# Performance work log

Measured on AMD Instinct MI355X. Metric: run time of the kernel, lower is better.

## Reference

```python
import jax, jax.numpy as jnp
import numpy as np

WINDOW_SIZE = 11
SIGMA = 1.5
C1 = 0.01 ** 2
C2 = 0.03 ** 2


def _gaussian_window(channels):
    coords = jnp.arange(WINDOW_SIZE, dtype=jnp.float32) - WINDOW_SIZE // 2
    g = jnp.exp(-coords ** 2 / (2.0 * SIGMA ** 2))
    g = g / g.sum()
    w2d = g[:, None] * g[None, :]                      # [K, K]
    # depthwise kernel: [out_ch=C, in_ch/groups=1, K, K]
    return jnp.broadcast_to(w2d[None, None], (channels, 1, WINDOW_SIZE, WINDOW_SIZE))


def _depthwise_conv(x, window):
    # x: [B, C, H, W]; grouped conv with feature_group_count = C, SAME padding
    C = x.shape[1]
    pad = WINDOW_SIZE // 2
    return jax.lax.conv_general_dilated(
        x, window,
        window_strides=(1, 1),
        padding=((pad, pad), (pad, pad)),
        dimension_numbers=("NCHW", "OIHW", "NCHW"),
        feature_group_count=C,
    )


def setup_inputs() -> dict:
    key = jax.random.key(0)
    k1, k2 = jax.random.split(key)
    shape = (16, 3, 512, 512)
    pred = jax.random.uniform(k1, shape, dtype=jnp.float32)
    target = jax.random.uniform(k2, shape, dtype=jnp.float32)
    return {"pred": pred, "target": target}


def reference(pred, target):
    C = pred.shape[1]
    window = _gaussian_window(C)
    mu_p = _depthwise_conv(pred, window)
    mu_t = _depthwise_conv(target, window)
    mu_p_sq = mu_p ** 2
    mu_t_sq = mu_t ** 2
    mu_cross = mu_p * mu_t
    sigma_p_sq = _depthwise_conv(pred ** 2, window) - mu_p_sq
    sigma_t_sq = _depthwise_conv(target ** 2, window) - mu_t_sq
    sigma_cross = _depthwise_conv(pred * target, window) - mu_cross
    ssim_map = ((2.0 * mu_cross + C1) * (2.0 * sigma_cross + C2)) / (
        (mu_p_sq + mu_t_sq + C1) * (sigma_p_sq + sigma_t_sq + C2)
    )
    return 1.0 - ssim_map.mean()
```

## Files before the change

### kernel.cpp

```cpp
#include <hip/hip_runtime.h>

#define HH 512
#define WW 512
#define NPLANE 48
#define BY 128
#define CHK 16
#define NCH (BY / CHK)
#define SLOTS 40
#define KS 11

typedef __attribute__((ext_vector_type(8))) short short8;
typedef __attribute__((ext_vector_type(4))) float floatx4;
typedef __attribute__((ext_vector_type(2))) float float2v;
typedef __attribute__((ext_vector_type(2))) __bf16 bf16x2v;

__device__ inline unsigned pk2bf_rne(float a, float b) {
    union { float f; unsigned u; } ua, ub;
    ua.f = a; ub.f = b;
    unsigned lo = (ua.u + 0x7FFFu + ((ua.u >> 16) & 1u)) >> 16;
    unsigned hi = (ub.u + 0x7FFFu + ((ub.u >> 16) & 1u)) >> 16;
    return lo | (hi << 16);
}

__device__ inline unsigned pkbf(float a, float b) {
    float2v f = {a, b};
    bf16x2v v = __builtin_convertvector(f, bf16x2v);
    return __builtin_bit_cast(unsigned, v);
}

struct Raw { float4 p0, p1, t0, t1; };

__global__ __launch_bounds__(256, 4) void ssim_kernel(
    const float* __restrict__ pred, const float* __restrict__ target,
    float* __restrict__ ws_sum)
{
    __shared__ __align__(16) short ring[4][4][16][SLOTS];

    const int tid = threadIdx.x;
    const int wv = tid >> 6;
    const int lane = tid & 63;
    const int m = lane & 15;
    const int quad = lane >> 4;

    float wsum = 0.f;
#pragma unroll
    for (int k = 0; k < KS; ++k) {
        float d = (float)(k - 5);
        wsum += __expf(-d * d * (1.0f / 4.5f));
    }
    const float invs = 1.0f / wsum;

    short8 Wf;
    {
        union { short8 v; unsigned u[4]; } W;
#pragma unroll
        for (int jj = 0; jj < 4; ++jj) {
            float v0, v1;
            {
                int idx = quad * 8 + 2 * jj - m - 3;
                float d = (float)(idx - 5);
                v0 = (idx >= 0 && idx < KS) ? __expf(-d * d * (1.0f / 4.5f)) * invs : 0.f;
            }
            {
                int idx = quad * 8 + 2 * jj + 1 - m - 3;
                float d = (float)(idx - 5);
                v1 = (idx >= 0 && idx < KS) ? __expf(-d * d * (1.0f / 4.5f)) * invs : 0.f;
            }
            W.u[jj] = pk2bf_rne(v0, v1);
        }
        Wf = W.v;
    }

    const size_t poff = (size_t)blockIdx.z * HH * WW;
    const float* __restrict__ pp = pred + poff;
    const float* __restrict__ tp = target + poff;
    const int X0 = blockIdx.x * 64 + wv * 16;
    const int rawX = X0 - 8;
    const int Y0 = blockIdx.y * BY;

    const float C1 = 1.0e-4f;
    const float C2 = 9.0e-4f;
    float lsum = 0.f;
    const floatx4 z = {0.f, 0.f, 0.f, 0.f};

    auto load_raw = [&](int k) -> Raw {
        Raw r;
        r.p0 = make_float4(0, 0, 0, 0); r.p1 = make_float4(0, 0, 0, 0);
        r.t0 = make_float4(0, 0, 0, 0); r.t1 = make_float4(0, 0, 0, 0);
        const int row = Y0 + CHK * k - 8 + m;
        if ((unsigned)row < (unsigned)HH) {
            const float* pr = pp + (size_t)row * WW;
            const float* tr = tp + (size_t)row * WW;
            const int c0 = rawX + quad * 8;
            if ((unsigned)c0 < (unsigned)WW) {
                r.p0 = *(const float4*)(pr + c0);
                r.t0 = *(const float4*)(tr + c0);
            }
            if ((unsigned)(c0 + 4) < (unsigned)WW) {
                r.p1 = *(const float4*)(pr + c0 + 4);
                r.t1 = *(const float4*)(tr + c0 + 4);
            }
        }
        return r;
    };

    auto h_step = [&](const Raw& r, int sb) {
        const float p[8] = {r.p0.x, r.p0.y, r.p0.z, r.p0.w,
                            r.p1.x, r.p1.y, r.p1.z, r.p1.w};
        const float t[8] = {r.t0.x, r.t0.y, r.t0.z, r.t0.w,
                            r.t1.x, r.t1.y, r.t1.z, r.t1.w};
        union { short8 v; unsigned u[4]; } Fp, Ft, Fq, Fpt;
#pragma unroll
        for (int jj = 0; jj < 4; ++jj) {
            const float a0 = p[2 * jj], a1 = p[2 * jj + 1];
            const float b0 = t[2 * jj], b1 = t[2 * jj + 1];
            Fp.u[jj]  = pkbf(a0, a1);
            Ft.u[jj]  = pkbf(b0, b1);
            Fq.u[jj]  = pkbf(fmaf(a0, a0, b0 * b0), fmaf(a1, a1, b1 * b1));
            Fpt.u[jj] = pkbf(a0 * b0, a1 * b1);
        }
        floatx4 Dp  = __builtin_amdgcn_mfma_f32_16x16x32_bf16(Fp.v,  Wf, z, 0, 0, 0);
        floatx4 Dt  = __builtin_amdgcn_mfma_f32_16x16x32_bf16(Ft.v,  Wf, z, 0, 0, 0);
        floatx4 Dq  = __builtin_amdgcn_mfma_f32_16x16x32_bf16(Fq.v,  Wf, z, 0, 0, 0);
        floatx4 Dpt = __builtin_amdgcn_mfma_f32_16x16x32_bf16(Fpt.v, Wf, z, 0, 0, 0);
        int slot = sb + quad * 4;
        if (slot >= SLOTS) slot -= SLOTS;
        uint2 v;
        v.x = pkbf(Dp[0], Dp[1]);   v.y = pkbf(Dp[2], Dp[3]);
        *(uint2*)&ring[wv][0][m][slot] = v;
        v.x = pkbf(Dt[0], Dt[1]);   v.y = pkbf(Dt[2], Dt[3]);
        *(uint2*)&ring[wv][1][m][slot] = v;
        v.x = pkbf(Dq[0], Dq[1]);   v.y = pkbf(Dq[2], Dq[3]);
        *(uint2*)&ring[wv][2][m][slot] = v;
        v.x = pkbf(Dpt[0], Dpt[1]); v.y = pkbf(Dpt[2], Dpt[3]);
        *(uint2*)&ring[wv][3][m][slot] = v;
    };

    Raw A = load_raw(0);
    Raw B = load_raw(1);
    Raw C = load_raw(2);
    Raw D = load_raw(3);
    h_step(A, (0 * CHK + SLOTS - 8) % SLOTS);
    h_step(B, (1 * CHK + SLOTS - 8) % SLOTS);
    int hb = (2 * CHK + SLOTS - 8) % SLOTS;
    int vb = SLOTS - 8;
#pragma unroll 1
    for (int i = 0; i < NCH; ++i) {
        int sq = vb + quad * 8;
        if (sq >= SLOTS) sq -= SLOTS;
        const short8 Bp  = *(const short8*)&ring[wv][0][m][sq];
        const short8 Bt  = *(const short8*)&ring[wv][1][m][sq];
        const short8 Bq  = *(const short8*)&ring[wv][2][m][sq];
        const short8 Bpt = *(const short8*)&ring[wv][3][m][sq];
        vb += CHK; if (vb >= SLOTS) vb -= SLOTS;

        if (i + 2 <= NCH) {
            h_step(C, hb);
            hb += CHK; if (hb >= SLOTS) hb -= SLOTS;
            C = D;
        }
        if (i + 4 <= NCH) D = load_raw(i + 4);

        floatx4 Mp  = __builtin_amdgcn_mfma_f32_16x16x32_bf16(Wf, Bp,  z, 0, 0, 0);
        floatx4 Mt  = __builtin_amdgcn_mfma_f32_16x16x32_bf16(Wf, Bt,  z, 0, 0, 0);
        floatx4 Mq  = __builtin_amdgcn_mfma_f32_16x16x32_bf16(Wf, Bq,  z, 0, 0, 0);
        floatx4 Mpt = __builtin_amdgcn_mfma_f32_16x16x32_bf16(Wf, Bpt, z, 0, 0, 0);
#pragma unroll
        for (int r = 0; r < 4; ++r) {
            const float mup = Mp[r], mut = Mt[r];
            const float mupsq = mup * mup, mutsq = mut * mut, mucr = mup * mut;
            const float scr = Mpt[r] - mucr;
            const float n1 = 2.f * mucr + C1;
            const float n2 = 2.f * scr + C2;
            const float d1 = mupsq + mutsq + C1;
            const float d2 = (Mq[r] - mupsq - mutsq) + C2;
            lsum += __fdividef(n1 * n2, d1 * d2);
        }
    }

#pragma unroll
    for (int off = 32; off > 0; off >>= 1) lsum += __shfl_down(lsum, off, 64);
    if (lane == 0) *(float*)&ring[wv][0][0][0] = lsum;
    __syncthreads();
    if (tid == 0) {
        atomicAdd(ws_sum, *(const float*)&ring[0][0][0][0]
                        + *(const float*)&ring[1][0][0][0]
                        + *(const float*)&ring[2][0][0][0]
                        + *(const float*)&ring[3][0][0][0]);
    }
}

__global__ void finalize_kernel(const float* __restrict__ ws_sum,
                                float* __restrict__ out) {
    out[0] = 1.0f - ws_sum[0] * (1.0f / 12582912.0f);
}

extern "C" void kernel_launch(void* const* d_in, const int* in_sizes, int n_in,
                              void* d_out, int out_size, void* d_ws, size_t ws_size,
                              hipStream_t stream) {
    const float* pred = (const float*)d_in[0];
    const float* target = (const float*)d_in[1];
    float* out = (float*)d_out;
    float* ws = (float*)d_ws;

    hipMemsetAsync(ws, 0, sizeof(float), stream);
    dim3 grid(WW / 64, HH / BY, NPLANE);
    ssim_kernel<<<grid, 256, 0, stream>>>(pred, target, ws);
    finalize_kernel<<<1, 1, 0, stream>>>(ws, out);
}
```

Before: 141.5 us.

## Shrink LDS ring to power-of-two, unroll pipeline by two, pack float2 math

Reduces the per-wave LDS ring from 40 to 32 slots so slot indices use a mask instead of a compare-and-subtract, and raises the launch-bounds occupancy hint from 4 to 6 blocks. The main loop is unrolled by two with fixed ring offsets and explicit prologue and epilogue steps, and row/column address and bounds checks are hoisted. The elementwise products and the SSIM epilogue now use float2 vector operations, so the compiler can emit packed FP32 instructions. The tighter register budget from the higher occupancy hint could cause spills, and the smaller ring must still leave room for every row the vertical pass reads.

```diff
diff --git a/kernel.cpp b/kernel.cpp
--- a/kernel.cpp
+++ b/kernel.cpp
@@ -6,7 +6,7 @@
 #define BY 128
 #define CHK 16
 #define NCH (BY / CHK)
-#define SLOTS 40
+#define SLOTS 32
 #define KS 11
 
 typedef __attribute__((ext_vector_type(8))) short short8;
@@ -22,15 +22,14 @@
     return lo | (hi << 16);
 }
 
-__device__ inline unsigned pkbf(float a, float b) {
-    float2v f = {a, b};
+__device__ inline unsigned pkbf2(float2v f) {
     bf16x2v v = __builtin_convertvector(f, bf16x2v);
     return __builtin_bit_cast(unsigned, v);
 }
 
 struct Raw { float4 p0, p1, t0, t1; };
 
-__global__ __launch_bounds__(256, 4) void ssim_kernel(
+__global__ __launch_bounds__(256, 6) void ssim_kernel(
     const float* __restrict__ pred, const float* __restrict__ target,
     float* __restrict__ ws_sum)
 {
@@ -72,14 +71,18 @@
     }
 
     const size_t poff = (size_t)blockIdx.z * HH * WW;
-    const float* __restrict__ pp = pred + poff;
-    const float* __restrict__ tp = target + poff;
     const int X0 = blockIdx.x * 64 + wv * 16;
     const int rawX = X0 - 8;
     const int Y0 = blockIdx.y * BY;
 
-    const float C1 = 1.0e-4f;
-    const float C2 = 9.0e-4f;
+    const int c0 = rawX + quad * 8;
+    const bool okc0 = (unsigned)c0 < (unsigned)WW;
+    const bool okc1 = (unsigned)(c0 + 4) < (unsigned)WW;
+    const float* __restrict__ pc = pred + poff + c0;
+    const float* __restrict__ tc = target + poff + c0;
+
+    const float2v C1v = {1.0e-4f, 1.0e-4f};
+    const float2v C2v = {9.0e-4f, 9.0e-4f};
     float lsum = 0.f;
     const floatx4 z = {0.f, 0.f, 0.f, 0.f};
 
@@ -89,94 +92,100 @@
         r.t0 = make_float4(0, 0, 0, 0); r.t1 = make_float4(0, 0, 0, 0);
         const int row = Y0 + CHK * k - 8 + m;
         if ((unsigned)row < (unsigned)HH) {
-            const float* pr = pp + (size_t)row * WW;
-            const float* tr = tp + (size_t)row * WW;
-            const int c0 = rawX + quad * 8;
-            if ((unsigned)c0 < (unsigned)WW) {
-                r.p0 = *(const float4*)(pr + c0);
-                r.t0 = *(const float4*)(tr + c0);
-            }
-            if ((unsigned)(c0 + 4) < (unsigned)WW) {
-                r.p1 = *(const float4*)(pr + c0 + 4);
-                r.t1 = *(const float4*)(tr + c0 + 4);
-            }
+            const float* pr = pc + (size_t)row * WW;
+            const float* tr = tc + (size_t)row * WW;
+            if (okc0) { r.p0 = *(const float4*)pr;      r.t0 = *(const float4*)tr; }
+            if (okc1) { r.p1 = *(const float4*)(pr + 4); r.t1 = *(const float4*)(tr + 4); }
         }
         return r;
     };
 
     auto h_step = [&](const Raw& r, int sb) {
-        const float p[8] = {r.p0.x, r.p0.y, r.p0.z, r.p0.w,
-                            r.p1.x, r.p1.y, r.p1.z, r.p1.w};
-        const float t[8] = {r.t0.x, r.t0.y, r.t0.z, r.t0.w,
-                            r.t1.x, r.t1.y, r.t1.z, r.t1.w};
+        const float2v pa[4] = {{r.p0.x, r.p0.y}, {r.p0.z, r.p0.w},
+                               {r.p1.x, r.p1.y}, {r.p1.z, r.p1.w}};
+        const float2v tb[4] = {{r.t0.x, r.t0.y}, {r.t0.z, r.t0.w},
+                               {r.t1.x, r.t1.y}, {r.t1.z, r.t1.w}};
         union { short8 v; unsigned u[4]; } Fp, Ft, Fq, Fpt;
 #pragma unroll
         for (int jj = 0; jj < 4; ++jj) {
-            const float a0 = p[2 * jj], a1 = p[2 * jj + 1];
-            const float b0 = t[2 * jj], b1 = t[2 * jj + 1];
-            Fp.u[jj]  = pkbf(a0, a1);
-            Ft.u[jj]  = pkbf(b0, b1);
-            Fq.u[jj]  = pkbf(fmaf(a0, a0, b0 * b0), fmaf(a1, a1, b1 * b1));
-            Fpt.u[jj] = pkbf(a0 * b0, a1 * b1);
+            Fp.u[jj]  = pkbf2(pa[jj]);
+            Ft.u[jj]  = pkbf2(tb[jj]);
+            Fq.u[jj]  = pkbf2(pa[jj] * pa[jj] + tb[jj] * tb[jj]);
+            Fpt.u[jj] = pkbf2(pa[jj] * tb[jj]);
         }
         floatx4 Dp  = __builtin_amdgcn_mfma_f32_16x16x32_bf16(Fp.v,  Wf, z, 0, 0, 0);
         floatx4 Dt  = __builtin_amdgcn_mfma_f32_16x16x32_bf16(Ft.v,  Wf, z, 0, 0, 0);
         floatx4 Dq  = __builtin_amdgcn_mfma_f32_16x16x32_bf16(Fq.v,  Wf, z, 0, 0, 0);
         floatx4 Dpt = __builtin_amdgcn_mfma_f32_16x16x32_bf16(Fpt.v, Wf, z, 0, 0, 0);
-        int slot = sb + quad * 4;
-        if (slot >= SLOTS) slot -= SLOTS;
+        const int slot = (sb + quad * 4) & (SLOTS - 1);
         uint2 v;
-        v.x = pkbf(Dp[0], Dp[1]);   v.y = pkbf(Dp[2], Dp[3]);
+        v.x = pkbf2(float2v{Dp[0],  Dp[1]});  v.y = pkbf2(float2v{Dp[2],  Dp[3]});
         *(uint2*)&ring[wv][0][m][slot] = v;
-        v.x = pkbf(Dt[0], Dt[1]);   v.y = pkbf(Dt[2], Dt[3]);
+        v.x = pkbf2(float2v{Dt[0],  Dt[1]});  v.y = pkbf2(float2v{Dt[2],  Dt[3]});
         *(uint2*)&ring[wv][1][m][slot] = v;
-        v.x = pkbf(Dq[0], Dq[1]);   v.y = pkbf(Dq[2], Dq[3]);
+        v.x = pkbf2(float2v{Dq[0],  Dq[1]});  v.y = pkbf2(float2v{Dq[2],  Dq[3]});
         *(uint2*)&ring[wv][2][m][slot] = v;
-        v.x = pkbf(Dpt[0], Dpt[1]); v.y = pkbf(Dpt[2], Dpt[3]);
+        v.x = pkbf2(float2v{Dpt[0], Dpt[1]}); v.y = pkbf2(float2v{Dpt[2], Dpt[3]});
         *(uint2*)&ring[wv][3][m][slot] = v;
     };
 
-    Raw A = load_raw(0);
-    Raw B = load_raw(1);
-    Raw C = load_raw(2);
-    Raw D = load_raw(3);
-    h_step(A, (0 * CHK + SLOTS - 8) % SLOTS);
-    h_step(B, (1 * CHK + SLOTS - 8) % SLOTS);
-    int hb = (2 * CHK + SLOTS - 8) % SLOTS;
-    int vb = SLOTS - 8;
-#pragma unroll 1
-    for (int i = 0; i < NCH; ++i) {
-        int sq = vb + quad * 8;
-        if (sq >= SLOTS) sq -= SLOTS;
-        const short8 Bp  = *(const short8*)&ring[wv][0][m][sq];
-        const short8 Bt  = *(const short8*)&ring[wv][1][m][sq];
-        const short8 Bq  = *(const short8*)&ring[wv][2][m][sq];
-        const short8 Bpt = *(const short8*)&ring[wv][3][m][sq];
-        vb += CHK; if (vb >= SLOTS) vb -= SLOTS;
-
-        if (i + 2 <= NCH) {
-            h_step(C, hb);
-            hb += CHK; if (hb >= SLOTS) hb -= SLOTS;
-            C = D;
-        }
-        if (i + 4 <= NCH) D = load_raw(i + 4);
-
+    short8 Bp, Bt, Bq, Bpt;
+    auto vread = [&](int base) {
+        const int sq = (base + quad * 8) & (SLOTS - 1);
+        Bp  = *(const short8*)&ring[wv][0][m][sq];
+        Bt  = *(const short8*)&ring[wv][1][m][sq];
+        Bq  = *(const short8*)&ring[wv][2][m][sq];
+        Bpt = *(const short8*)&ring[wv][3][m][sq];
+    };
+
+    auto vfin = [&]() {
         floatx4 Mp  = __builtin_amdgcn_mfma_f32_16x16x32_bf16(Wf, Bp,  z, 0, 0, 0);
         floatx4 Mt  = __builtin_amdgcn_mfma_f32_16x16x32_bf16(Wf, Bt,  z, 0, 0, 0);
         floatx4 Mq  = __builtin_amdgcn_mfma_f32_16x16x32_bf16(Wf, Bq,  z, 0, 0, 0);
         floatx4 Mpt = __builtin_amdgcn_mfma_f32_16x16x32_bf16(Wf, Bpt, z, 0, 0, 0);
 #pragma unroll
-        for (int r = 0; r < 4; ++r) {
-            const float mup = Mp[r], mut = Mt[r];
-            const float mupsq = mup * mup, mutsq = mut * mut, mucr = mup * mut;
-            const float scr = Mpt[r] - mucr;
-            const float n1 = 2.f * mucr + C1;
-            const float n2 = 2.f * scr + C2;
-            const float d1 = mupsq + mutsq + C1;
-            const float d2 = (Mq[r] - mupsq - mutsq) + C2;
-            lsum += __fdividef(n1 * n2, d1 * d2);
-        }
-    }
+        for (int h = 0; h < 2; ++h) {
+            const float2v mup = {Mp[2*h],  Mp[2*h+1]};
+            const float2v mut = {Mt[2*h],  Mt[2*h+1]};
+            const float2v mq  = {Mq[2*h],  Mq[2*h+1]};
+            const float2v mpt = {Mpt[2*h], Mpt[2*h+1]};
+            const float2v mupsq = mup * mup, mutsq = mut * mut, mucr = mup * mut;
+            const float2v scr = mpt - mucr;
+            const float2v n1 = mucr + mucr + C1v;
+            const float2v n2 = scr + scr + C2v;
+            const float2v d1 = mupsq + mutsq + C1v;
+            const float2v d2 = (mq - mupsq - mutsq) + C2v;
+            const float2v num = n1 * n2, den = d1 * d2;
+            lsum += __fdividef(num[0], den[0]) + __fdividef(num[1], den[1]);
+        }
+    };
+
+    {
+        Raw A = load_raw(0);
+        Raw B = load_raw(1);
+        h_step(A, 24);
+        h_step(B, 8);
+    }
+    Raw C = load_raw(2);
+    Raw D = load_raw(3);
+
+#pragma unroll 1
+    for (int ii = 0; ii < 6; ii += 2) {
+        vread(24);
+        h_step(C, 24);
+        C = load_raw(ii + 4);
+        vfin();
+
+        vread(8);
+        h_step(D, 8);
+        if (ii < 4) D = load_raw(ii + 5);
+        vfin();
+    }
+    vread(24);
+    h_step(C, 24);
+    vfin();
+    vread(8);
+    vfin();
 
 #pragma unroll
     for (int off = 32; off > 0; off >>= 1) lsum += __shfl_down(lsum, off, 64);
```

Result: slower. 166.3 us (+17.6%).
